# Kernel optimization log

Measured on AMD Instinct MI355X. Metric: run time of the kernel, lower is better.

The kernel has to match this reference:

```python
import jax, jax.numpy as jnp
import numpy as np

HIDDEN = 1024
N_HEAD = 16
LN_EPS = 1e-5


def _layernorm(x, g, b):
    m = jnp.mean(x, axis=-1, keepdims=True)
    v = jnp.var(x, axis=-1, keepdims=True)
    return (x - m) * jax.lax.rsqrt(v + LN_EPS) * g + b


def setup_inputs() -> dict:
    key = jax.random.key(0)
    ks = jax.random.split(key, 16)
    H = HIDDEN
    s = 0.02
    d = dict(
        x=jax.random.normal(ks[0], (4, 1024, H), jnp.float32),
        Wq=jax.random.normal(ks[1], (H, H), jnp.float32) * s,
        bq=jnp.zeros((H,), jnp.float32),
        Wk=jax.random.normal(ks[2], (H, H), jnp.float32) * s,
        bk=jnp.zeros((H,), jnp.float32),
        Wv=jax.random.normal(ks[3], (H, H), jnp.float32) * s,
        bv=jnp.zeros((H,), jnp.float32),
        Wo=jax.random.normal(ks[4], (H, H), jnp.float32) * s,
        bo=jnp.zeros((H,), jnp.float32),
        g1=jax.random.normal(ks[5], (H,), jnp.float32) * s,
        b1=jnp.zeros((H,), jnp.float32),
        W1=jax.random.normal(ks[6], (H, 4 * H), jnp.float32) * s,
        c1=jnp.zeros((4 * H,), jnp.float32),
        W2=jax.random.normal(ks[7], (4 * H, H), jnp.float32) * s,
        c2=jnp.zeros((H,), jnp.float32),
        g2=jax.random.normal(ks[8], (H,), jnp.float32) * s,
        b2=jnp.zeros((H,), jnp.float32),
    )
    return d


def reference(x, Wq, bq, Wk, bk, Wv, bv, Wo, bo, g1, b1, W1, c1, W2, c2, g2, b2):
    N, T, Hd = x.shape
    Hh = N_HEAD
    D = Hd // Hh
    # faithful to torch code: .view(N, H, T, D) is a raw reshape, no transpose
    q = (x @ Wq + bq).reshape(N, Hh, T, D)
    k = (x @ Wk + bk).reshape(N, Hh, T, D)
    v = (x @ Wv + bv).reshape(N, Hh, T, D)
    scores = jnp.einsum('nhtd,nhsd->nhts', q, k) / jnp.sqrt(jnp.float32(Hd))
    # faithful: softmax over dim=1 (the head axis)
    attn = jax.nn.softmax(scores, axis=1)
    o = jnp.einsum('nhts,nhsd->nhtd', attn, v).reshape(N, T, Hd)
    o = o @ Wo + bo
    x1 = _layernorm(o + x, g1, b1)
    ff = jax.nn.gelu(x1 @ W1 + c1, approximate=False) @ W2 + c2
    return _layernorm(ff + x1, g2, b2)
```

## Files before the change

kernel.cpp:

```cpp
#include <hip/hip_runtime.h>
#include <cstdint>
#include <cstddef>

#define EPI_QKV  0
#define EPI_F32  2
#define EPI_GELU 3
#define EPI_PART 4

typedef __attribute__((ext_vector_type(8))) short bfrag8;
typedef __attribute__((ext_vector_type(4))) float facc4;

struct PtrQuad { unsigned short* p[4]; };

__device__ __forceinline__ unsigned short f2b(float x) {
  unsigned int u = __builtin_bit_cast(unsigned int, x);
  u += 0x7FFFu + ((u >> 16) & 1u);
  return (unsigned short)(u >> 16);
}
__device__ __forceinline__ float b2f(unsigned short u) {
  unsigned int x = ((unsigned int)u) << 16;
  return __builtin_bit_cast(float, x);
}

__device__ __forceinline__ void gl2lds16(const unsigned short* g, unsigned short* l) {
  __builtin_amdgcn_global_load_lds(
      (const __attribute__((address_space(1))) unsigned int*)g,
      (__attribute__((address_space(3))) unsigned int*)l, 16, 0, 0);
}

__global__ __launch_bounds__(256)
void cvt_bf16_kernel(const float* __restrict__ in, unsigned short* __restrict__ out, int n4) {
  const int i = blockIdx.x * 256 + threadIdx.x;
  if (i < n4) {
    const float4 v = ((const float4*)in)[i];
    ushort4 u;
    u.x = f2b(v.x); u.y = f2b(v.y); u.z = f2b(v.z); u.w = f2b(v.w);
    ((ushort4*)out)[i] = u;
  }
}

__global__ __launch_bounds__(256)
void transpose_cvt(const float* __restrict__ in, unsigned short* __restrict__ out,
                   int K, int N) {
  __shared__ float tile[32][33];
  const int n0 = blockIdx.x * 32;
  const int k0 = blockIdx.y * 32;
  const int tx = threadIdx.x & 31, ty = threadIdx.x >> 5;
#pragma unroll
  for (int i = 0; i < 32; i += 8)
    tile[ty + i][tx] = in[(size_t)(k0 + ty + i) * N + n0 + tx];
  __syncthreads();
#pragma unroll
  for (int i = 0; i < 32; i += 8)
    out[(size_t)(n0 + ty + i) * K + k0 + tx] = f2b(tile[tx][ty + i]);
}

template<int EPI>
__global__ __launch_bounds__(256, 2)
void gemm_bt(const unsigned short* __restrict__ A,
             const unsigned short* __restrict__ Bt,
             const float* __restrict__ bias,
             const float* __restrict__ bias2,
             const float* __restrict__ bias3,
             void* __restrict__ out, PtrQuad pq,
             int M, int N, int K, int ldk) {
  __shared__ unsigned short sA[128 * 32];
  __shared__ unsigned short sB[128 * 32];
  const int tid  = threadIdx.x;
  const int lane = tid & 63;
  const int wave = tid >> 6;
  const int l15  = lane & 15, l4 = lane >> 4;
  const int wr = wave >> 1, wc = wave & 1;
  const long row0 = (long)blockIdx.y * 128;
  const long col0 = (long)blockIdx.x * 128;
  const long k0   = (long)blockIdx.z * K;

  facc4 acc[4][4];
#pragma unroll
  for (int i = 0; i < 4; i++)
#pragma unroll
    for (int j = 0; j < 4; j++) acc[i][j] = (facc4)0.f;

  const int srow = tid >> 2;
  const int scol = (tid & 3) * 8;
  const unsigned short* Ap0 = A  + (row0 + srow) * (long)ldk + k0 + scol;
  const unsigned short* Ap1 = Ap0 + 64 * (long)ldk;
  const unsigned short* Bp0 = Bt + (col0 + srow) * (long)ldk + k0 + scol;
  const unsigned short* Bp1 = Bp0 + 64 * (long)ldk;
  const int wbase = (tid & ~63) * 8;
  unsigned short* sA0 = &sA[wbase];
  unsigned short* sA1 = &sA[2048 + wbase];
  unsigned short* sB0 = &sB[wbase];
  unsigned short* sB1 = &sB[2048 + wbase];

  const int aoff = (wr * 64 + l15) * 32 + l4 * 8;
  const int boff = (wc * 64 + l15) * 32 + l4 * 8;

  for (int kt = 0; kt < K; kt += 32) {
    gl2lds16(Ap0 + kt, sA0);
    gl2lds16(Ap1 + kt, sA1);
    gl2lds16(Bp0 + kt, sB0);
    gl2lds16(Bp1 + kt, sB1);
    __syncthreads();
    bfrag8 af[4], bf[4];
#pragma unroll
    for (int i = 0; i < 4; i++) af[i] = *(const bfrag8*)&sA[aoff + i * 512];
#pragma unroll
    for (int j = 0; j < 4; j++) bf[j] = *(const bfrag8*)&sB[boff + j * 512];
#pragma unroll
    for (int i = 0; i < 4; i++)
#pragma unroll
      for (int j = 0; j < 4; j++)
        acc[i][j] = __builtin_amdgcn_mfma_f32_16x16x32_bf16(af[i], bf[j], acc[i][j], 0, 0, 0);
    __syncthreads();
  }

#pragma unroll
  for (int i = 0; i < 4; i++) {
    const long m0 = row0 + wr * 64 + i * 16 + l4 * 4;
#pragma unroll
    for (int j = 0; j < 4; j++) {
      const long c = col0 + wc * 64 + j * 16 + l15;
      if constexpr (EPI == EPI_QKV) {
        const long which = c >> 10;
        const long cl = c & 1023;
        unsigned short* oq = (unsigned short*)out;
        if (which == 0) {
          const float bj = bias[cl];
#pragma unroll
          for (int r = 0; r < 4; r++)
            oq[(m0 + r) * 1024 + cl] = f2b((acc[i][j][r] + bj) * 0.03125f);
        } else if (which == 1) {
          const float bj = bias2[cl];
#pragma unroll
          for (int r = 0; r < 4; r++)
            (oq + 4194304)[(m0 + r) * 1024 + cl] = f2b(acc[i][j][r] + bj);
        } else {
          const float bj = bias3[cl];
          const long cc = cl >> 6, d = cl & 63;
#pragma unroll
          for (int r = 0; r < 4; r++) {
            const long m = m0 + r;
            const long nbb = m >> 10, rr = m & 1023;
            const long h = rr >> 6, rhi = rr & 63;
            const long s = rhi * 16 + cc;
            (oq + 8388608)[((nbb * 16 + h) * 64 + d) * 1024 + s] = f2b(acc[i][j][r] + bj);
          }
        }
      } else if constexpr (EPI == EPI_F32) {
        const float bj = bias[c];
        float* of = (float*)out;
#pragma unroll
        for (int r = 0; r < 4; r++) of[(m0 + r) * (long)N + c] = acc[i][j][r] + bj;
      } else if constexpr (EPI == EPI_PART) {
        unsigned short* ob = pq.p[blockIdx.z];
#pragma unroll
        for (int r = 0; r < 4; r++) ob[(m0 + r) * (long)N + c] = f2b(acc[i][j][r]);
      } else {
        const float bj = bias[c];
        unsigned short* ob = (unsigned short*)out;
#pragma unroll
        for (int r = 0; r < 4; r++) {
          const float t = acc[i][j][r] + bj;
          ob[(m0 + r) * (long)N + c] = f2b(0.5f * t * (1.f + erff(t * 0.70710678f)));
        }
      }
    }
  }
}

__global__ __launch_bounds__(512, 4)
void attn_kernel(const unsigned short* __restrict__ Qb,
                 const unsigned short* __restrict__ Kb,
                 const unsigned short* __restrict__ Vt,
                 unsigned short* __restrict__ P0, unsigned short* __restrict__ P1) {
  const int id = blockIdx.x;
  const int combo = id & 7;
  const int tile = id >> 3;
  const int nb = combo & 3;
  const int sp = combo >> 2;
  const int tid = threadIdx.x, lane = tid & 63;
  const int w = __builtin_amdgcn_readfirstlane(tid >> 6);
  const int l15 = lane & 15, l4 = lane >> 4;
  const int t0 = tile * 16;

  __shared__ float red[2][8][576];
  __shared__ __align__(16) unsigned short abuf[8][16][40];

  const size_t hb0 = (size_t)(nb * 16 + w * 2) << 16;
  const unsigned short* qB = Qb + hb0;
  const unsigned short* kB = Kb + hb0;
  const unsigned short* vB = Vt + hb0;

  bfrag8 qf[2][2];
#pragma unroll
  for (int hh = 0; hh < 2; hh++)
#pragma unroll
    for (int ks = 0; ks < 2; ks++)
      qf[hh][ks] = *(const bfrag8*)(qB + (hh << 16) + (t0 + l15) * 64 + ks * 32 + l4 * 8);

  facc4 oacc[2][4];
#pragma unroll
  for (int hh = 0; hh < 2; hh++)
#pragma unroll
    for (int nt = 0; nt < 4; nt++) oacc[hh][nt] = (facc4)0.f;

  for (int it = 0; it < 16; ++it) {
    const int s0 = sp * 512 + it * 32;
    const int pb = it & 1;
    facc4 sacc[2][2];
#pragma unroll
    for (int hh = 0; hh < 2; hh++)
#pragma unroll
      for (int nt = 0; nt < 2; nt++) sacc[hh][nt] = (facc4)0.f;
#pragma unroll
    for (int hh = 0; hh < 2; hh++) {
      const unsigned short* kh = kB + (hh << 16);
#pragma unroll
      for (int ks = 0; ks < 2; ks++)
#pragma unroll
        for (int nt = 0; nt < 2; nt++) {
          const bfrag8 kf = *(const bfrag8*)(kh + (s0 + nt * 16 + l15) * 64 + ks * 32 + l4 * 8);
          sacc[hh][nt] = __builtin_amdgcn_mfma_f32_16x16x32_bf16(qf[hh][ks], kf, sacc[hh][nt], 0, 0, 0);
        }
    }
    bfrag8 vf0[4], vf1[4];
#pragma unroll
    for (int nt = 0; nt < 4; nt++) {
      vf0[nt] = *(const bfrag8*)(vB + (size_t)(nt * 16 + l15) * 1024 + s0 + l4 * 8);
      vf1[nt] = *(const bfrag8*)(vB + (1 << 16) + (size_t)(nt * 16 + l15) * 1024 + s0 + l4 * 8);
    }
#pragma unroll
    for (int nt = 0; nt < 2; nt++)
#pragma unroll
      for (int r = 0; r < 4; r++) {
        const float e0 = __expf(sacc[0][nt][r]);
        const float e1 = __expf(sacc[1][nt][r]);
        sacc[0][nt][r] = e0; sacc[1][nt][r] = e1;
        red[pb][w][(l4 * 4 + r) * 36 + nt * 16 + l15] = e0 + e1;
      }
    __syncthreads();
    float rinv[2][4];
#pragma unroll
    for (int nt = 0; nt < 2; nt++)
#pragma unroll
      for (int r = 0; r < 4; r++) {
        const int o = (l4 * 4 + r) * 36 + nt * 16 + l15;
        float s = 0.f;
#pragma unroll
        for (int ww = 0; ww < 8; ww++) s += red[pb][ww][o];
        rinv[nt][r] = 1.f / s;
      }
#pragma unroll
    for (int nt = 0; nt < 2; nt++)
#pragma unroll
      for (int r = 0; r < 4; r++)
        abuf[w][l4 * 4 + r][nt * 16 + l15] = f2b(sacc[0][nt][r] * rinv[nt][r]);
    {
      const bfrag8 af0 = *(const bfrag8*)&abuf[w][l15][l4 * 8];
#pragma unroll
      for (int nt = 0; nt < 4; nt++)
        oacc[0][nt] = __builtin_amdgcn_mfma_f32_16x16x32_bf16(af0, vf0[nt], oacc[0][nt], 0, 0, 0);
    }
#pragma unroll
    for (int nt = 0; nt < 2; nt++)
#pragma unroll
      for (int r = 0; r < 4; r++)
        abuf[w][l4 * 4 + r][nt * 16 + l15] = f2b(sacc[1][nt][r] * rinv[nt][r]);
    {
      const bfrag8 af1 = *(const bfrag8*)&abuf[w][l15][l4 * 8];
#pragma unroll
      for (int nt = 0; nt < 4; nt++)
        oacc[1][nt] = __builtin_amdgcn_mfma_f32_16x16x32_bf16(af1, vf1[nt], oacc[1][nt], 0, 0, 0);
    }
  }
  unsigned short* P = sp ? P1 : P0;
#pragma unroll
  for (int hh = 0; hh < 2; hh++) {
    const size_t rb = ((size_t)nb * 1024 + (size_t)(w * 2 + hh) * 64 + tile) * 1024;
#pragma unroll
    for (int nt = 0; nt < 4; nt++)
#pragma unroll
      for (int r = 0; r < 4; r++)
        P[rb + (size_t)(l4 * 4 + r) * 64 + nt * 16 + l15] = f2b(oacc[hh][nt][r]);
  }
}

__global__ __launch_bounds__(256)
void reduce_o2(const unsigned short* __restrict__ P0, const unsigned short* __restrict__ P1,
               unsigned short* __restrict__ OB, int n4) {
  const int i = blockIdx.x * 256 + threadIdx.x;
  if (i < n4) {
    const ushort4 a = ((const ushort4*)P0)[i];
    const ushort4 b = ((const ushort4*)P1)[i];
    ushort4 u;
    u.x = f2b(b2f(a.x) + b2f(b.x));
    u.y = f2b(b2f(a.y) + b2f(b.y));
    u.z = f2b(b2f(a.z) + b2f(b.z));
    u.w = f2b(b2f(a.w) + b2f(b.w));
    ((ushort4*)OB)[i] = u;
  }
}

__global__ __launch_bounds__(256)
void ln_red(const unsigned short* __restrict__ P0, const unsigned short* __restrict__ P1,
            const unsigned short* __restrict__ P2, const unsigned short* __restrict__ P3,
            const float* __restrict__ bias, const float* __restrict__ resid,
            const float* __restrict__ g, const float* __restrict__ be,
            float* __restrict__ outf, unsigned short* __restrict__ outb) {
  const int row = blockIdx.x, tid = threadIdx.x;
  const size_t o4 = (size_t)row * 256 + tid;
  const ushort4 a = ((const ushort4*)P0)[o4];
  const ushort4 b = ((const ushort4*)P1)[o4];
  const ushort4 c = ((const ushort4*)P2)[o4];
  const ushort4 d = ((const ushort4*)P3)[o4];
  const float4 vb = ((const float4*)bias)[tid];
  const float4 vr = ((const float4*)resid)[o4];
  float t0 = b2f(a.x) + b2f(b.x) + b2f(c.x) + b2f(d.x) + vb.x + vr.x;
  float t1 = b2f(a.y) + b2f(b.y) + b2f(c.y) + b2f(d.y) + vb.y + vr.y;
  float t2 = b2f(a.z) + b2f(b.z) + b2f(c.z) + b2f(d.z) + vb.z + vr.z;
  float t3 = b2f(a.w) + b2f(b.w) + b2f(c.w) + b2f(d.w) + vb.w + vr.w;
  float s = t0 + t1 + t2 + t3;
  float q = t0 * t0 + t1 * t1 + t2 * t2 + t3 * t3;
#pragma unroll
  for (int off = 32; off > 0; off >>= 1) {
    s += __shfl_down(s, off, 64);
    q += __shfl_down(q, off, 64);
  }
  __shared__ float rs_[4], rq_[4];
  if ((tid & 63) == 0) { rs_[tid >> 6] = s; rq_[tid >> 6] = q; }
  __syncthreads();
  const float S = rs_[0] + rs_[1] + rs_[2] + rs_[3];
  const float Q = rq_[0] + rq_[1] + rq_[2] + rq_[3];
  const float mean = S * (1.f / 1024.f);
  const float var  = Q * (1.f / 1024.f) - mean * mean;
  const float rstd = rsqrtf(var + 1e-5f);
  const float4 vg  = ((const float4*)g)[tid];
  const float4 vbe = ((const float4*)be)[tid];
  float o0 = (t0 - mean) * rstd * vg.x + vbe.x;
  float o1 = (t1 - mean) * rstd * vg.y + vbe.y;
  float o2 = (t2 - mean) * rstd * vg.z + vbe.z;
  float o3 = (t3 - mean) * rstd * vg.w + vbe.w;
  ((float4*)(outf + (size_t)row * 1024))[tid] = make_float4(o0, o1, o2, o3);
  if (outb != nullptr) {
    ushort4 u;
    u.x = f2b(o0); u.y = f2b(o1); u.z = f2b(o2); u.w = f2b(o3);
    ((ushort4*)(outb + (size_t)row * 1024))[tid] = u;
  }
}

extern "C" void kernel_launch(void* const* d_in, const int* in_sizes, int n_in,
                              void* d_out, int out_size, void* d_ws, size_t ws_size,
                              hipStream_t stream) {
  const float* x  = (const float*)d_in[0];
  const float* Wq = (const float*)d_in[1];
  const float* bq = (const float*)d_in[2];
  const float* Wk = (const float*)d_in[3];
  const float* bk = (const float*)d_in[4];
  const float* Wv = (const float*)d_in[5];
  const float* bv = (const float*)d_in[6];
  const float* Wo = (const float*)d_in[7];
  const float* bo = (const float*)d_in[8];
  const float* g1 = (const float*)d_in[9];
  const float* b1 = (const float*)d_in[10];
  const float* W1 = (const float*)d_in[11];
  const float* c1 = (const float*)d_in[12];
  const float* W2 = (const float*)d_in[13];
  const float* c2 = (const float*)d_in[14];
  const float* g2 = (const float*)d_in[15];
  const float* b2 = (const float*)d_in[16];
  float* out = (float*)d_out;

  char* ws = (char*)d_ws;
  unsigned short* XB  = (unsigned short*)(ws);
  unsigned short* WQT = (unsigned short*)(ws + 8388608);
  unsigned short* WKT = (unsigned short*)(ws + 10485760);
  unsigned short* WVT = (unsigned short*)(ws + 12582912);
  unsigned short* WOT = (unsigned short*)(ws + 14680064);
  unsigned short* W1T = (unsigned short*)(ws + 16777216);
  unsigned short* W2T = (unsigned short*)(ws + 25165824);
  float*          X1  = (float*)(ws + 33554432);
  unsigned short* X1B = (unsigned short*)(ws + 50331648);
  char* RB = ws + 58720256;
  unsigned short* QB  = (unsigned short*)(RB);
  unsigned short* KB  = (unsigned short*)(RB + 8388608);
  unsigned short* VT  = (unsigned short*)(RB + 16777216);
  unsigned short* OB  = (unsigned short*)(RB + 25165824);
  unsigned short* H1B = (unsigned short*)(RB);
  unsigned short* AP0 = (unsigned short*)(RB + 33554432);
  unsigned short* AP1 = (unsigned short*)(RB + 41943040);
  PtrQuad OPQ = { { QB, KB, VT, XB } };
  PtrQuad FPQ = { { XB, X1B, (unsigned short*)(RB + 33554432),
                    (unsigned short*)(RB + 41943040) } };
  PtrQuad ZQ = { { nullptr, nullptr, nullptr, nullptr } };

  const dim3 tb(256);
  cvt_bf16_kernel<<<dim3(4096), tb, 0, stream>>>(x, XB, 1048576);
  transpose_cvt<<<dim3(32, 32),  tb, 0, stream>>>(Wq, WQT, 1024, 1024);
  transpose_cvt<<<dim3(32, 32),  tb, 0, stream>>>(Wk, WKT, 1024, 1024);
  transpose_cvt<<<dim3(32, 32),  tb, 0, stream>>>(Wv, WVT, 1024, 1024);
  transpose_cvt<<<dim3(32, 32),  tb, 0, stream>>>(Wo, WOT, 1024, 1024);
  transpose_cvt<<<dim3(128, 32), tb, 0, stream>>>(W1, W1T, 1024, 4096);
  transpose_cvt<<<dim3(32, 128), tb, 0, stream>>>(W2, W2T, 4096, 1024);
  gemm_bt<EPI_QKV><<<dim3(24, 32), tb, 0, stream>>>(XB, WQT, bq, bk, bv, (void*)QB, ZQ,
                                                    4096, 3072, 1024, 1024);
  attn_kernel<<<dim3(512), dim3(512), 0, stream>>>(QB, KB, VT, AP0, AP1);
  reduce_o2<<<dim3(4096), tb, 0, stream>>>(AP0, AP1, OB, 1048576);
  gemm_bt<EPI_PART><<<dim3(8, 32, 4), tb, 0, stream>>>(OB, WOT, nullptr, nullptr, nullptr,
                                                       nullptr, OPQ, 4096, 1024, 256, 1024);
  ln_red<<<dim3(4096), tb, 0, stream>>>(QB, KB, VT, XB, bo, x, g1, b1, X1, X1B);
  gemm_bt<EPI_GELU><<<dim3(32, 32), tb, 0, stream>>>(X1B, W1T, c1, nullptr, nullptr,
                                                     (void*)H1B, ZQ, 4096, 4096, 1024, 1024);
  gemm_bt<EPI_PART><<<dim3(8, 32, 4), tb, 0, stream>>>(H1B, W2T, nullptr, nullptr, nullptr,
                                                       nullptr, FPQ, 4096, 1024, 1024, 4096);
  ln_red<<<dim3(4096), tb, 0, stream>>>(FPQ.p[0], FPQ.p[1], FPQ.p[2], FPQ.p[3], c2, X1,
                                        g2, b2, out, (unsigned short*)nullptr);
}
```

Before: 463.0 us.

## Restructure head-axis softmax attention to keep all heads per wave in registers

The attention kernel is reorganised so each wave computes scores for all 16 heads over its own 16-key slice, and the head-axis softmax is reduced entirely in registers instead of through a cross-wave LDS reduction. Q for a 32-row tile is staged once into swizzled LDS and reused across heads. Normalised probabilities are exchanged through an LDS buffer so each wave can run P·V for its two heads over a 128-key step. Tiles double to 32 query rows and the grid is halved, which raises register pressure (occupancy hint lowered to 2) and adds several barriers per iteration.

```diff
diff --git a/kernel.cpp b/kernel.cpp
--- a/kernel.cpp
+++ b/kernel.cpp
@@ -169,120 +169,161 @@
   }
 }
 
-__global__ __launch_bounds__(512, 4)
+__global__ __launch_bounds__(512, 2)
 void attn_kernel(const unsigned short* __restrict__ Qb,
                  const unsigned short* __restrict__ Kb,
                  const unsigned short* __restrict__ Vt,
                  unsigned short* __restrict__ P0, unsigned short* __restrict__ P1) {
   const int id = blockIdx.x;
   const int combo = id & 7;
-  const int tile = id >> 3;
   const int nb = combo & 3;
   const int sp = combo >> 2;
+  const int tile = id >> 3;
   const int tid = threadIdx.x, lane = tid & 63;
   const int w = __builtin_amdgcn_readfirstlane(tid >> 6);
   const int l15 = lane & 15, l4 = lane >> 4;
-  const int t0 = tile * 16;
-
-  __shared__ float red[2][8][576];
-  __shared__ __align__(16) unsigned short abuf[8][16][40];
-
-  const size_t hb0 = (size_t)(nb * 16 + w * 2) << 16;
-  const unsigned short* qB = Qb + hb0;
-  const unsigned short* kB = Kb + hb0;
-  const unsigned short* vB = Vt + hb0;
-
-  bfrag8 qf[2][2];
+  const int t0 = tile * 32;
+  const int sbase = sp * 512;
+
+  __shared__ __align__(16) unsigned short Qs[16 * 32 * 64];
+  __shared__ __align__(16) unsigned short Ps[16 * 16 * 128];
+
+  const size_t bb = ((size_t)(nb * 16)) << 16;
+  const unsigned short* qB = Qb + bb;
+  const unsigned short* kB = Kb + bb;
+  const unsigned short* vB = Vt + bb;
+
+#pragma unroll
+  for (int kk = 0; kk < 8; kk++) {
+    const int j = kk * 512 + tid;
+    const int h = j >> 8, t = (j >> 3) & 31, d8 = j & 7;
+    const int4 v = *(const int4*)(qB + ((size_t)h << 16) + (size_t)(t0 + t) * 64 + d8 * 8);
+    *(int4*)((char*)Qs + h * 4096 + t * 128 + ((d8 * 16) ^ ((t & 7) << 4))) = v;
+  }
+
+  const int swz = (l15 & 7) << 4;
+  const int qrA = l15 * 128;
+  const int qrB = (16 + l15) * 128;
+  const int qo0 = (l4 * 16) ^ swz;
+  const int qo1 = (64 + l4 * 16) ^ swz;
+  const int pwb = l15 * 256 + (((w * 16 + l4 * 4) * 2) ^ swz);
+  int pro[4];
+#pragma unroll
+  for (int ks = 0; ks < 4; ks++) pro[ks] = l15 * 256 + ((ks * 64 + l4 * 16) ^ swz);
+
+  const int h0 = w * 2;
+  facc4 oacc[2][2][4];
 #pragma unroll
   for (int hh = 0; hh < 2; hh++)
 #pragma unroll
-    for (int ks = 0; ks < 2; ks++)
-      qf[hh][ks] = *(const bfrag8*)(qB + (hh << 16) + (t0 + l15) * 64 + ks * 32 + l4 * 8);
-
-  facc4 oacc[2][4];
-#pragma unroll
-  for (int hh = 0; hh < 2; hh++)
-#pragma unroll
-    for (int nt = 0; nt < 4; nt++) oacc[hh][nt] = (facc4)0.f;
-
-  for (int it = 0; it < 16; ++it) {
-    const int s0 = sp * 512 + it * 32;
-    const int pb = it & 1;
-    facc4 sacc[2][2];
+    for (int st = 0; st < 2; st++)
+#pragma unroll
+      for (int nt = 0; nt < 4; nt++) oacc[hh][st][nt] = (facc4)0.f;
+
+  __syncthreads();
+
+  for (int it = 0; it < 4; ++it) {
+    const int s0w = sbase + it * 128 + w * 16;
+    facc4 scA[16], scB[16];
+#pragma unroll
+    for (int h = 0; h < 16; h++) {
+      const unsigned short* kh = kB + ((size_t)h << 16) + (size_t)(s0w + l15) * 64 + l4 * 8;
+      const bfrag8 kf0 = *(const bfrag8*)kh;
+      const bfrag8 kf1 = *(const bfrag8*)(kh + 32);
+      const char* qh = (const char*)Qs + h * 4096;
+      const bfrag8 qA0 = *(const bfrag8*)(qh + qrA + qo0);
+      const bfrag8 qA1 = *(const bfrag8*)(qh + qrA + qo1);
+      const bfrag8 qB0 = *(const bfrag8*)(qh + qrB + qo0);
+      const bfrag8 qB1 = *(const bfrag8*)(qh + qrB + qo1);
+      facc4 a = __builtin_amdgcn_mfma_f32_16x16x32_bf16(kf0, qA0, (facc4)0.f, 0, 0, 0);
+      scA[h] = __builtin_amdgcn_mfma_f32_16x16x32_bf16(kf1, qA1, a, 0, 0, 0);
+      facc4 b = __builtin_amdgcn_mfma_f32_16x16x32_bf16(kf0, qB0, (facc4)0.f, 0, 0, 0);
+      scB[h] = __builtin_amdgcn_mfma_f32_16x16x32_bf16(kf1, qB1, b, 0, 0, 0);
+    }
+    {
+      float d0 = 0.f, d1 = 0.f, d2 = 0.f, d3 = 0.f;
+#pragma unroll
+      for (int h = 0; h < 16; h++) {
+        scA[h][0] = __expf(scA[h][0]); d0 += scA[h][0];
+        scA[h][1] = __expf(scA[h][1]); d1 += scA[h][1];
+        scA[h][2] = __expf(scA[h][2]); d2 += scA[h][2];
+        scA[h][3] = __expf(scA[h][3]); d3 += scA[h][3];
+      }
+      const float r0 = 1.f / d0, r1 = 1.f / d1, r2 = 1.f / d2, r3 = 1.f / d3;
+#pragma unroll
+      for (int h = 0; h < 16; h++) {
+        const float p0 = scA[h][0] * r0, p1 = scA[h][1] * r1;
+        const float p2 = scA[h][2] * r2, p3 = scA[h][3] * r3;
+        uint2 pk;
+        asm("v_cvt_pk_bf16_f32 %0, %1, %2" : "=v"(pk.x) : "v"(p0), "v"(p1));
+        asm("v_cvt_pk_bf16_f32 %0, %1, %2" : "=v"(pk.y) : "v"(p2), "v"(p3));
+        *(uint2*)((char*)Ps + h * 4096 + pwb) = pk;
+      }
+    }
+    __syncthreads();
+    bfrag8 afA[2][4];
 #pragma unroll
     for (int hh = 0; hh < 2; hh++)
 #pragma unroll
-      for (int nt = 0; nt < 2; nt++) sacc[hh][nt] = (facc4)0.f;
+      for (int ks = 0; ks < 4; ks++)
+        afA[hh][ks] = *(const bfrag8*)((char*)Ps + (h0 + hh) * 4096 + pro[ks]);
+    __syncthreads();
+    {
+      float d0 = 0.f, d1 = 0.f, d2 = 0.f, d3 = 0.f;
+#pragma unroll
+      for (int h = 0; h < 16; h++) {
+        scB[h][0] = __expf(scB[h][0]); d0 += scB[h][0];
+        scB[h][1] = __expf(scB[h][1]); d1 += scB[h][1];
+        scB[h][2] = __expf(scB[h][2]); d2 += scB[h][2];
+        scB[h][3] = __expf(scB[h][3]); d3 += scB[h][3];
+      }
+      const float r0 = 1.f / d0, r1 = 1.f / d1, r2 = 1.f / d2, r3 = 1.f / d3;
+#pragma unroll
+      for (int h = 0; h < 16; h++) {
+        const float p0 = scB[h][0] * r0, p1 = scB[h][1] * r1;
+        const float p2 = scB[h][2] * r2, p3 = scB[h][3] * r3;
+        uint2 pk;
+        asm("v_cvt_pk_bf16_f32 %0, %1, %2" : "=v"(pk.x) : "v"(p0), "v"(p1));
+        asm("v_cvt_pk_bf16_f32 %0, %1, %2" : "=v"(pk.y) : "v"(p2), "v"(p3));
+        *(uint2*)((char*)Ps + h * 4096 + pwb) = pk;
+      }
+    }
+    __syncthreads();
+    bfrag8 afB[2][4];
+#pragma unroll
+    for (int hh = 0; hh < 2; hh++)
+#pragma unroll
+      for (int ks = 0; ks < 4; ks++)
+        afB[hh][ks] = *(const bfrag8*)((char*)Ps + (h0 + hh) * 4096 + pro[ks]);
+    __syncthreads();
 #pragma unroll
     for (int hh = 0; hh < 2; hh++) {
-      const unsigned short* kh = kB + (hh << 16);
-#pragma unroll
-      for (int ks = 0; ks < 2; ks++)
-#pragma unroll
-        for (int nt = 0; nt < 2; nt++) {
-          const bfrag8 kf = *(const bfrag8*)(kh + (s0 + nt * 16 + l15) * 64 + ks * 32 + l4 * 8);
-          sacc[hh][nt] = __builtin_amdgcn_mfma_f32_16x16x32_bf16(qf[hh][ks], kf, sacc[hh][nt], 0, 0, 0);
+      const unsigned short* vh = vB + ((size_t)(h0 + hh) << 16) + sbase + it * 128 + l4 * 8;
+#pragma unroll
+      for (int ks = 0; ks < 4; ks++)
+#pragma unroll
+        for (int nt = 0; nt < 4; nt++) {
+          const bfrag8 vf = *(const bfrag8*)(vh + (size_t)(nt * 16 + l15) * 1024 + ks * 32);
+          oacc[hh][0][nt] =
+              __builtin_amdgcn_mfma_f32_16x16x32_bf16(afA[hh][ks], vf, oacc[hh][0][nt], 0, 0, 0);
+          oacc[hh][1][nt] =
+              __builtin_amdgcn_mfma_f32_16x16x32_bf16(afB[hh][ks], vf, oacc[hh][1][nt], 0, 0, 0);
         }
     }
-    bfrag8 vf0[4], vf1[4];
-#pragma unroll
-    for (int nt = 0; nt < 4; nt++) {
-      vf0[nt] = *(const bfrag8*)(vB + (size_t)(nt * 16 + l15) * 1024 + s0 + l4 * 8);
-      vf1[nt] = *(const bfrag8*)(vB + (1 << 16) + (size_t)(nt * 16 + l15) * 1024 + s0 + l4 * 8);
-    }
-#pragma unroll
-    for (int nt = 0; nt < 2; nt++)
-#pragma unroll
-      for (int r = 0; r < 4; r++) {
-        const float e0 = __expf(sacc[0][nt][r]);
-        const float e1 = __expf(sacc[1][nt][r]);
-        sacc[0][nt][r] = e0; sacc[1][nt][r] = e1;
-        red[pb][w][(l4 * 4 + r) * 36 + nt * 16 + l15] = e0 + e1;
-      }
-    __syncthreads();
-    float rinv[2][4];
-#pragma unroll
-    for (int nt = 0; nt < 2; nt++)
-#pragma unroll
-      for (int r = 0; r < 4; r++) {
-        const int o = (l4 * 4 + r) * 36 + nt * 16 + l15;
-        float s = 0.f;
-#pragma unroll
-        for (int ww = 0; ww < 8; ww++) s += red[pb][ww][o];
-        rinv[nt][r] = 1.f / s;
-      }
-#pragma unroll
-    for (int nt = 0; nt < 2; nt++)
-#pragma unroll
-      for (int r = 0; r < 4; r++)
-        abuf[w][l4 * 4 + r][nt * 16 + l15] = f2b(sacc[0][nt][r] * rinv[nt][r]);
-    {
-      const bfrag8 af0 = *(const bfrag8*)&abuf[w][l15][l4 * 8];
+  }
+
+  unsigned short* P = sp ? P1 : P0;
+#pragma unroll
+  for (int hh = 0; hh < 2; hh++) {
+    const size_t hb = ((size_t)nb << 20) + ((size_t)(h0 + hh) << 16);
+#pragma unroll
+    for (int st = 0; st < 2; st++)
 #pragma unroll
       for (int nt = 0; nt < 4; nt++)
-        oacc[0][nt] = __builtin_amdgcn_mfma_f32_16x16x32_bf16(af0, vf0[nt], oacc[0][nt], 0, 0, 0);
-    }
-#pragma unroll
-    for (int nt = 0; nt < 2; nt++)
-#pragma unroll
-      for (int r = 0; r < 4; r++)
-        abuf[w][l4 * 4 + r][nt * 16 + l15] = f2b(sacc[1][nt][r] * rinv[nt][r]);
-    {
-      const bfrag8 af1 = *(const bfrag8*)&abuf[w][l15][l4 * 8];
-#pragma unroll
-      for (int nt = 0; nt < 4; nt++)
-        oacc[1][nt] = __builtin_amdgcn_mfma_f32_16x16x32_bf16(af1, vf1[nt], oacc[1][nt], 0, 0, 0);
-    }
-  }
-  unsigned short* P = sp ? P1 : P0;
-#pragma unroll
-  for (int hh = 0; hh < 2; hh++) {
-    const size_t rb = ((size_t)nb * 1024 + (size_t)(w * 2 + hh) * 64 + tile) * 1024;
-#pragma unroll
-    for (int nt = 0; nt < 4; nt++)
-#pragma unroll
-      for (int r = 0; r < 4; r++)
-        P[rb + (size_t)(l4 * 4 + r) * 64 + nt * 16 + l15] = f2b(oacc[hh][nt][r]);
+#pragma unroll
+        for (int r = 0; r < 4; r++)
+          P[hb + (size_t)(t0 + st * 16 + l4 * 4 + r) * 64 + nt * 16 + l15] =
+              f2b(oacc[hh][st][nt][r]);
   }
 }
 
@@ -404,7 +445,7 @@
   transpose_cvt<<<dim3(32, 128), tb, 0, stream>>>(W2, W2T, 4096, 1024);
   gemm_bt<EPI_QKV><<<dim3(24, 32), tb, 0, stream>>>(XB, WQT, bq, bk, bv, (void*)QB, ZQ,
                                                     4096, 3072, 1024, 1024);
-  attn_kernel<<<dim3(512), dim3(512), 0, stream>>>(QB, KB, VT, AP0, AP1);
+  attn_kernel<<<dim3(256), dim3(512), 0, stream>>>(QB, KB, VT, AP0, AP1);
   reduce_o2<<<dim3(4096), tb, 0, stream>>>(AP0, AP1, OB, 1048576);
   gemm_bt<EPI_PART><<<dim3(8, 32, 4), tb, 0, stream>>>(OB, WOT, nullptr, nullptr, nullptr,
                                                        nullptr, OPQ, 4096, 1024, 256, 1024);
```

After: 423.4 us. -8.5%, faster.

## Restructure attention kernel with head-split QK and LDS-staged probabilities

Applied to the files above, without the earlier changes.

Reorganizes the attention kernel so each warp computes scores for 8 heads over a 16-key sub-slice, and Q is staged once in swizzled LDS. The head-axis softmax denominator is combined across just two warp groups instead of eight. Probabilities are packed to bf16 with a hardware convert instruction and exchanged through LDS so each warp then runs PV for its own 2 heads over 64 keys per iteration. This halves the iteration count and cuts reduction traffic, at the cost of an extra barrier per iteration and larger LDS use. The output write indexing also changes, which may alter the layout handed to the reduction stage.

```diff
diff --git a/kernel.cpp b/kernel.cpp
--- a/kernel.cpp
+++ b/kernel.cpp
@@ -176,113 +176,124 @@
                  unsigned short* __restrict__ P0, unsigned short* __restrict__ P1) {
   const int id = blockIdx.x;
   const int combo = id & 7;
-  const int tile = id >> 3;
   const int nb = combo & 3;
   const int sp = combo >> 2;
+  const int tile = id >> 3;
   const int tid = threadIdx.x, lane = tid & 63;
   const int w = __builtin_amdgcn_readfirstlane(tid >> 6);
   const int l15 = lane & 15, l4 = lane >> 4;
   const int t0 = tile * 16;
-
-  __shared__ float red[2][8][576];
-  __shared__ __align__(16) unsigned short abuf[8][16][40];
-
-  const size_t hb0 = (size_t)(nb * 16 + w * 2) << 16;
-  const unsigned short* qB = Qb + hb0;
-  const unsigned short* kB = Kb + hb0;
-  const unsigned short* vB = Vt + hb0;
-
-  bfrag8 qf[2][2];
+  const int sbase = sp * 512;
+
+  __shared__ __align__(16) unsigned short Qs[16 * 16 * 64];
+  __shared__ __align__(16) unsigned short Ps[16 * 16 * 64];
+  __shared__ __align__(16) float Ds[2 * 16 * 64];
+
+  const size_t bb = ((size_t)(nb * 16)) << 16;
+  const unsigned short* qB = Qb + bb;
+  const unsigned short* kB = Kb + bb;
+  const unsigned short* vB = Vt + bb;
+
+#pragma unroll
+  for (int kk = 0; kk < 4; kk++) {
+    const int j = kk * 512 + tid;
+    const int h = j >> 7, t = (j >> 3) & 15, d8 = j & 7;
+    const int4 v = *(const int4*)(qB + ((size_t)h << 16) + (size_t)(t0 + t) * 64 + d8 * 8);
+    *(int4*)((char*)Qs + h * 2048 + t * 128 + ((d8 * 16) ^ ((t & 7) << 4))) = v;
+  }
+
+  const int g   = w & 1;
+  const int sw  = w >> 1;
+  const int h0q = g * 8;
+  const int hpv = w * 2;
+  const int swz = (l15 & 7) << 4;
+
+  const int qrow = l15 * 128;
+  const int qo0 = (l4 * 16) ^ swz;
+  const int qo1 = (64 + l4 * 16) ^ swz;
+  const int pwb = l15 * 128 + ((sw * 32 + l4 * 8) ^ swz);
+  const int pr0 = l15 * 128 + ((l4 * 16) ^ swz);
+  const int pr1 = l15 * 128 + ((64 + l4 * 16) ^ swz);
+  const int dwo = l15 * 256 + ((sw * 64 + l4 * 16) ^ swz);
+
+  facc4 oacc[2][4];
 #pragma unroll
   for (int hh = 0; hh < 2; hh++)
 #pragma unroll
-    for (int ks = 0; ks < 2; ks++)
-      qf[hh][ks] = *(const bfrag8*)(qB + (hh << 16) + (t0 + l15) * 64 + ks * 32 + l4 * 8);
-
-  facc4 oacc[2][4];
-#pragma unroll
-  for (int hh = 0; hh < 2; hh++)
-#pragma unroll
     for (int nt = 0; nt < 4; nt++) oacc[hh][nt] = (facc4)0.f;
 
-  for (int it = 0; it < 16; ++it) {
-    const int s0 = sp * 512 + it * 32;
-    const int pb = it & 1;
-    facc4 sacc[2][2];
-#pragma unroll
-    for (int hh = 0; hh < 2; hh++)
-#pragma unroll
-      for (int nt = 0; nt < 2; nt++) sacc[hh][nt] = (facc4)0.f;
+  __syncthreads();
+
+  for (int it = 0; it < 8; ++it) {
+    const int s0 = sbase + it * 64;
+    const int sW = s0 + sw * 16;
+    facc4 sc[8];
+#pragma unroll
+    for (int hi = 0; hi < 8; hi++) {
+      const int h = h0q + hi;
+      const unsigned short* kh = kB + ((size_t)h << 16) + (size_t)(sW + l15) * 64 + l4 * 8;
+      const bfrag8 kf0 = *(const bfrag8*)kh;
+      const bfrag8 kf1 = *(const bfrag8*)(kh + 32);
+      const char* qh = (const char*)Qs + h * 2048 + qrow;
+      const bfrag8 q0 = *(const bfrag8*)(qh + qo0);
+      const bfrag8 q1 = *(const bfrag8*)(qh + qo1);
+      facc4 a = __builtin_amdgcn_mfma_f32_16x16x32_bf16(kf0, q0, (facc4)0.f, 0, 0, 0);
+      sc[hi] = __builtin_amdgcn_mfma_f32_16x16x32_bf16(kf1, q1, a, 0, 0, 0);
+    }
+    float d0 = 0.f, d1 = 0.f, d2 = 0.f, d3 = 0.f;
+#pragma unroll
+    for (int hi = 0; hi < 8; hi++) {
+      sc[hi][0] = __expf(sc[hi][0]); d0 += sc[hi][0];
+      sc[hi][1] = __expf(sc[hi][1]); d1 += sc[hi][1];
+      sc[hi][2] = __expf(sc[hi][2]); d2 += sc[hi][2];
+      sc[hi][3] = __expf(sc[hi][3]); d3 += sc[hi][3];
+    }
+    *(float4*)((char*)Ds + g * 4096 + dwo) = make_float4(d0, d1, d2, d3);
+    __syncthreads();
+    const float4 dp = *(const float4*)((char*)Ds + (g ^ 1) * 4096 + dwo);
+    const float r0 = 1.f / (d0 + dp.x);
+    const float r1 = 1.f / (d1 + dp.y);
+    const float r2 = 1.f / (d2 + dp.z);
+    const float r3 = 1.f / (d3 + dp.w);
+#pragma unroll
+    for (int hi = 0; hi < 8; hi++) {
+      const float p0 = sc[hi][0] * r0, p1 = sc[hi][1] * r1;
+      const float p2 = sc[hi][2] * r2, p3 = sc[hi][3] * r3;
+      uint2 pk;
+      asm("v_cvt_pk_bf16_f32 %0, %1, %2" : "=v"(pk.x) : "v"(p0), "v"(p1));
+      asm("v_cvt_pk_bf16_f32 %0, %1, %2" : "=v"(pk.y) : "v"(p2), "v"(p3));
+      *(uint2*)((char*)Ps + (h0q + hi) * 2048 + pwb) = pk;
+    }
+    __syncthreads();
+    bfrag8 af[2][2];
 #pragma unroll
     for (int hh = 0; hh < 2; hh++) {
-      const unsigned short* kh = kB + (hh << 16);
+      af[hh][0] = *(const bfrag8*)((char*)Ps + (hpv + hh) * 2048 + pr0);
+      af[hh][1] = *(const bfrag8*)((char*)Ps + (hpv + hh) * 2048 + pr1);
+    }
+#pragma unroll
+    for (int hh = 0; hh < 2; hh++) {
+      const unsigned short* vh = vB + ((size_t)(hpv + hh) << 16) + s0 + l4 * 8;
 #pragma unroll
       for (int ks = 0; ks < 2; ks++)
 #pragma unroll
-        for (int nt = 0; nt < 2; nt++) {
-          const bfrag8 kf = *(const bfrag8*)(kh + (s0 + nt * 16 + l15) * 64 + ks * 32 + l4 * 8);
-          sacc[hh][nt] = __builtin_amdgcn_mfma_f32_16x16x32_bf16(qf[hh][ks], kf, sacc[hh][nt], 0, 0, 0);
+        for (int nt = 0; nt < 4; nt++) {
+          const bfrag8 vf = *(const bfrag8*)(vh + (size_t)(nt * 16 + l15) * 1024 + ks * 32);
+          oacc[hh][nt] =
+              __builtin_amdgcn_mfma_f32_16x16x32_bf16(af[hh][ks], vf, oacc[hh][nt], 0, 0, 0);
         }
     }
-    bfrag8 vf0[4], vf1[4];
-#pragma unroll
-    for (int nt = 0; nt < 4; nt++) {
-      vf0[nt] = *(const bfrag8*)(vB + (size_t)(nt * 16 + l15) * 1024 + s0 + l4 * 8);
-      vf1[nt] = *(const bfrag8*)(vB + (1 << 16) + (size_t)(nt * 16 + l15) * 1024 + s0 + l4 * 8);
-    }
-#pragma unroll
-    for (int nt = 0; nt < 2; nt++)
-#pragma unroll
-      for (int r = 0; r < 4; r++) {
-        const float e0 = __expf(sacc[0][nt][r]);
-        const float e1 = __expf(sacc[1][nt][r]);
-        sacc[0][nt][r] = e0; sacc[1][nt][r] = e1;
-        red[pb][w][(l4 * 4 + r) * 36 + nt * 16 + l15] = e0 + e1;
-      }
-    __syncthreads();
-    float rinv[2][4];
-#pragma unroll
-    for (int nt = 0; nt < 2; nt++)
-#pragma unroll
-      for (int r = 0; r < 4; r++) {
-        const int o = (l4 * 4 + r) * 36 + nt * 16 + l15;
-        float s = 0.f;
-#pragma unroll
-        for (int ww = 0; ww < 8; ww++) s += red[pb][ww][o];
-        rinv[nt][r] = 1.f / s;
-      }
-#pragma unroll
-    for (int nt = 0; nt < 2; nt++)
+  }
+
+  unsigned short* P = sp ? P1 : P0;
+#pragma unroll
+  for (int hh = 0; hh < 2; hh++) {
+    const size_t hb = ((size_t)nb << 20) + ((size_t)(hpv + hh) << 16);
+#pragma unroll
+    for (int nt = 0; nt < 4; nt++)
 #pragma unroll
       for (int r = 0; r < 4; r++)
-        abuf[w][l4 * 4 + r][nt * 16 + l15] = f2b(sacc[0][nt][r] * rinv[nt][r]);
-    {
-      const bfrag8 af0 = *(const bfrag8*)&abuf[w][l15][l4 * 8];
-#pragma unroll
-      for (int nt = 0; nt < 4; nt++)
-        oacc[0][nt] = __builtin_amdgcn_mfma_f32_16x16x32_bf16(af0, vf0[nt], oacc[0][nt], 0, 0, 0);
-    }
-#pragma unroll
-    for (int nt = 0; nt < 2; nt++)
-#pragma unroll
-      for (int r = 0; r < 4; r++)
-        abuf[w][l4 * 4 + r][nt * 16 + l15] = f2b(sacc[1][nt][r] * rinv[nt][r]);
-    {
-      const bfrag8 af1 = *(const bfrag8*)&abuf[w][l15][l4 * 8];
-#pragma unroll
-      for (int nt = 0; nt < 4; nt++)
-        oacc[1][nt] = __builtin_amdgcn_mfma_f32_16x16x32_bf16(af1, vf1[nt], oacc[1][nt], 0, 0, 0);
-    }
-  }
-  unsigned short* P = sp ? P1 : P0;
-#pragma unroll
-  for (int hh = 0; hh < 2; hh++) {
-    const size_t rb = ((size_t)nb * 1024 + (size_t)(w * 2 + hh) * 64 + tile) * 1024;
-#pragma unroll
-    for (int nt = 0; nt < 4; nt++)
-#pragma unroll
-      for (int r = 0; r < 4; r++)
-        P[rb + (size_t)(l4 * 4 + r) * 64 + nt * 16 + l15] = f2b(oacc[hh][nt][r]);
+        P[hb + (size_t)(t0 + l4 * 4 + r) * 64 + nt * 16 + l15] = f2b(oacc[hh][nt][r]);
   }
 }
 
```

After: 461.5 us. Within noise of the previous version (-0.3%).

## Restructure attention kernel: 4 heads per wave, 64-row tiles, 4-way key split

Applied to the files above, without the earlier changes.

The attention kernel is reorganised so each wave handles 4 heads and 32 query rows. Blocks now cover 64 query rows with a 4-way split over keys instead of 2-way, which gives 256 blocks. The head-axis softmax denominator is partly summed in registers and only reduced across 4 head groups through LDS, instead of across 8 waves. The bf16 packing uses v_cvt_pk_bf16_f32 with an XOR-swizzled LDS layout, and the final reduction now sums 4 partial outputs. This is meant to increase reuse of loaded K/V fragments and cut LDS reduction traffic. In exchange it raises register pressure (launch bounds drop to 1 block), halves the grid, adds extra partial-buffer traffic, and reuses workspace regions (X1 area) for the partials.

```diff
diff --git a/kernel.cpp b/kernel.cpp
--- a/kernel.cpp
+++ b/kernel.cpp
@@ -169,135 +169,193 @@
   }
 }
 
-__global__ __launch_bounds__(512, 4)
+__global__ __launch_bounds__(512, 1)
 void attn_kernel(const unsigned short* __restrict__ Qb,
                  const unsigned short* __restrict__ Kb,
                  const unsigned short* __restrict__ Vt,
-                 unsigned short* __restrict__ P0, unsigned short* __restrict__ P1) {
+                 PtrQuad APQ) {
   const int id = blockIdx.x;
-  const int combo = id & 7;
-  const int tile = id >> 3;
+  const int combo = id & 15;
   const int nb = combo & 3;
   const int sp = combo >> 2;
+  const int tile = id >> 4;
   const int tid = threadIdx.x, lane = tid & 63;
   const int w = __builtin_amdgcn_readfirstlane(tid >> 6);
   const int l15 = lane & 15, l4 = lane >> 4;
-  const int t0 = tile * 16;
-
-  __shared__ float red[2][8][576];
-  __shared__ __align__(16) unsigned short abuf[8][16][40];
-
-  const size_t hb0 = (size_t)(nb * 16 + w * 2) << 16;
-  const unsigned short* qB = Qb + hb0;
-  const unsigned short* kB = Kb + hb0;
-  const unsigned short* vB = Vt + hb0;
-
-  bfrag8 qf[2][2];
-#pragma unroll
-  for (int hh = 0; hh < 2; hh++)
-#pragma unroll
-    for (int ks = 0; ks < 2; ks++)
-      qf[hh][ks] = *(const bfrag8*)(qB + (hh << 16) + (t0 + l15) * 64 + ks * 32 + l4 * 8);
-
-  facc4 oacc[2][4];
-#pragma unroll
-  for (int hh = 0; hh < 2; hh++)
-#pragma unroll
-    for (int nt = 0; nt < 4; nt++) oacc[hh][nt] = (facc4)0.f;
-
-  for (int it = 0; it < 16; ++it) {
-    const int s0 = sp * 512 + it * 32;
-    const int pb = it & 1;
-    facc4 sacc[2][2];
-#pragma unroll
-    for (int hh = 0; hh < 2; hh++)
-#pragma unroll
-      for (int nt = 0; nt < 2; nt++) sacc[hh][nt] = (facc4)0.f;
-#pragma unroll
-    for (int hh = 0; hh < 2; hh++) {
-      const unsigned short* kh = kB + (hh << 16);
-#pragma unroll
-      for (int ks = 0; ks < 2; ks++)
-#pragma unroll
-        for (int nt = 0; nt < 2; nt++) {
-          const bfrag8 kf = *(const bfrag8*)(kh + (s0 + nt * 16 + l15) * 64 + ks * 32 + l4 * 8);
-          sacc[hh][nt] = __builtin_amdgcn_mfma_f32_16x16x32_bf16(qf[hh][ks], kf, sacc[hh][nt], 0, 0, 0);
-        }
-    }
-    bfrag8 vf0[4], vf1[4];
-#pragma unroll
-    for (int nt = 0; nt < 4; nt++) {
-      vf0[nt] = *(const bfrag8*)(vB + (size_t)(nt * 16 + l15) * 1024 + s0 + l4 * 8);
-      vf1[nt] = *(const bfrag8*)(vB + (1 << 16) + (size_t)(nt * 16 + l15) * 1024 + s0 + l4 * 8);
-    }
-#pragma unroll
-    for (int nt = 0; nt < 2; nt++)
-#pragma unroll
-      for (int r = 0; r < 4; r++) {
-        const float e0 = __expf(sacc[0][nt][r]);
-        const float e1 = __expf(sacc[1][nt][r]);
-        sacc[0][nt][r] = e0; sacc[1][nt][r] = e1;
-        red[pb][w][(l4 * 4 + r) * 36 + nt * 16 + l15] = e0 + e1;
+  const int tg = w >> 2;
+  const int hg = w & 3;
+  const int t0 = tile * 64 + tg * 32;
+  const int h0 = hg * 4;
+  const int sbase = sp * 256;
+
+  __shared__ float Ds[2][2][4][32][33];
+  __shared__ __align__(16) unsigned short Pw[8][8][512];
+
+  const size_t bb = ((size_t)(nb * 16)) << 16;
+  const unsigned short* qB = Qb + bb;
+  const unsigned short* kB = Kb + bb;
+  const unsigned short* vB = Vt + bb;
+
+  bfrag8 qf[4][2][2];
+#pragma unroll
+  for (int hi = 0; hi < 4; hi++)
+#pragma unroll
+    for (int ts = 0; ts < 2; ts++)
+#pragma unroll
+      for (int dh = 0; dh < 2; dh++)
+        qf[hi][ts][dh] = *(const bfrag8*)(qB + ((size_t)(h0 + hi) << 16)
+            + (size_t)(t0 + ts * 16 + l15) * 64 + dh * 32 + l4 * 8);
+
+  facc4 oacc[4][2][4];
+#pragma unroll
+  for (int hi = 0; hi < 4; hi++)
+#pragma unroll
+    for (int ts = 0; ts < 2; ts++)
+#pragma unroll
+      for (int nt = 0; nt < 4; nt++) oacc[hi][ts][nt] = (facc4)0.f;
+
+  const int pswz = (l15 & 3) << 4;
+  char* pw = (char*)&Pw[w][0][0];
+
+  for (int it = 0; it < 8; ++it) {
+    const int s0 = sbase + it * 32;
+    bfrag8 kf[4][2][2];
+#pragma unroll
+    for (int hi = 0; hi < 4; hi++)
+#pragma unroll
+      for (int ss = 0; ss < 2; ss++)
+#pragma unroll
+        for (int dh = 0; dh < 2; dh++)
+          kf[hi][ss][dh] = *(const bfrag8*)(kB + ((size_t)(h0 + hi) << 16)
+              + (size_t)(s0 + ss * 16 + l15) * 64 + dh * 32 + l4 * 8);
+    facc4 sc[4][2][2];
+#pragma unroll
+    for (int hi = 0; hi < 4; hi++)
+#pragma unroll
+      for (int ts = 0; ts < 2; ts++)
+#pragma unroll
+        for (int ss = 0; ss < 2; ss++) {
+          facc4 a = __builtin_amdgcn_mfma_f32_16x16x32_bf16(kf[hi][ss][0], qf[hi][ts][0],
+                                                            (facc4)0.f, 0, 0, 0);
+          sc[hi][ts][ss] = __builtin_amdgcn_mfma_f32_16x16x32_bf16(kf[hi][ss][1],
+                                                                   qf[hi][ts][1], a, 0, 0, 0);
+        }
+    bfrag8 vf[4][4];
+#pragma unroll
+    for (int hi = 0; hi < 4; hi++)
+#pragma unroll
+      for (int nt = 0; nt < 4; nt++)
+        vf[hi][nt] = *(const bfrag8*)(vB + ((size_t)(h0 + hi) << 16)
+            + (size_t)(nt * 16 + l15) * 1024 + s0 + l4 * 8);
+    float dp[2][2][4];
+#pragma unroll
+    for (int ts = 0; ts < 2; ts++)
+#pragma unroll
+      for (int ss = 0; ss < 2; ss++)
+#pragma unroll
+        for (int r = 0; r < 4; r++) dp[ts][ss][r] = 0.f;
+#pragma unroll
+    for (int hi = 0; hi < 4; hi++)
+#pragma unroll
+      for (int ts = 0; ts < 2; ts++)
+#pragma unroll
+        for (int ss = 0; ss < 2; ss++)
+#pragma unroll
+          for (int r = 0; r < 4; r++) {
+            const float e = __expf(sc[hi][ts][ss][r]);
+            sc[hi][ts][ss][r] = e;
+            dp[ts][ss][r] += e;
+          }
+    const int p = it & 1;
+#pragma unroll
+    for (int ts = 0; ts < 2; ts++)
+#pragma unroll
+      for (int ss = 0; ss < 2; ss++)
+#pragma unroll
+        for (int r = 0; r < 4; r++)
+          Ds[p][tg][hg][ss * 16 + l4 * 4 + r][ts * 16 + l15] = dp[ts][ss][r];
+    __syncthreads();
+    float ri[2][2][4];
+#pragma unroll
+    for (int ts = 0; ts < 2; ts++)
+#pragma unroll
+      for (int ss = 0; ss < 2; ss++)
+#pragma unroll
+        for (int r = 0; r < 4; r++) {
+          const int si = ss * 16 + l4 * 4 + r;
+          const int ti = ts * 16 + l15;
+          float s = dp[ts][ss][r];
+          s += Ds[p][tg][(hg + 1) & 3][si][ti];
+          s += Ds[p][tg][(hg + 2) & 3][si][ti];
+          s += Ds[p][tg][(hg + 3) & 3][si][ti];
+          ri[ts][ss][r] = 1.f / s;
+        }
+#pragma unroll
+    for (int hi = 0; hi < 4; hi++)
+#pragma unroll
+      for (int ts = 0; ts < 2; ts++) {
+        uint2 a, b;
+        {
+          const float p0 = sc[hi][ts][0][0] * ri[ts][0][0];
+          const float p1 = sc[hi][ts][0][1] * ri[ts][0][1];
+          const float p2 = sc[hi][ts][0][2] * ri[ts][0][2];
+          const float p3 = sc[hi][ts][0][3] * ri[ts][0][3];
+          asm("v_cvt_pk_bf16_f32 %0, %1, %2" : "=v"(a.x) : "v"(p0), "v"(p1));
+          asm("v_cvt_pk_bf16_f32 %0, %1, %2" : "=v"(a.y) : "v"(p2), "v"(p3));
+        }
+        {
+          const float p0 = sc[hi][ts][1][0] * ri[ts][1][0];
+          const float p1 = sc[hi][ts][1][1] * ri[ts][1][1];
+          const float p2 = sc[hi][ts][1][2] * ri[ts][1][2];
+          const float p3 = sc[hi][ts][1][3] * ri[ts][1][3];
+          asm("v_cvt_pk_bf16_f32 %0, %1, %2" : "=v"(b.x) : "v"(p0), "v"(p1));
+          asm("v_cvt_pk_bf16_f32 %0, %1, %2" : "=v"(b.y) : "v"(p2), "v"(p3));
+        }
+        char* base = pw + (hi * 2 + ts) * 1024 + l15 * 64;
+        *(uint2*)(base + ((l4 * 8) ^ pswz)) = a;
+        *(uint2*)(base + ((32 + l4 * 8) ^ pswz)) = b;
       }
-    __syncthreads();
-    float rinv[2][4];
-#pragma unroll
-    for (int nt = 0; nt < 2; nt++)
-#pragma unroll
-      for (int r = 0; r < 4; r++) {
-        const int o = (l4 * 4 + r) * 36 + nt * 16 + l15;
-        float s = 0.f;
-#pragma unroll
-        for (int ww = 0; ww < 8; ww++) s += red[pb][ww][o];
-        rinv[nt][r] = 1.f / s;
+#pragma unroll
+    for (int hi = 0; hi < 4; hi++)
+#pragma unroll
+      for (int ts = 0; ts < 2; ts++) {
+        const bfrag8 af = *(const bfrag8*)(pw + (hi * 2 + ts) * 1024 + l15 * 64
+                                           + ((l4 * 16) ^ pswz));
+#pragma unroll
+        for (int nt = 0; nt < 4; nt++)
+          oacc[hi][ts][nt] = __builtin_amdgcn_mfma_f32_16x16x32_bf16(af, vf[hi][nt],
+                                                                     oacc[hi][ts][nt], 0, 0, 0);
       }
-#pragma unroll
-    for (int nt = 0; nt < 2; nt++)
-#pragma unroll
-      for (int r = 0; r < 4; r++)
-        abuf[w][l4 * 4 + r][nt * 16 + l15] = f2b(sacc[0][nt][r] * rinv[nt][r]);
-    {
-      const bfrag8 af0 = *(const bfrag8*)&abuf[w][l15][l4 * 8];
+  }
+
+  unsigned short* P = APQ.p[sp];
+#pragma unroll
+  for (int hi = 0; hi < 4; hi++) {
+    const size_t hb = ((size_t)nb << 20) + ((size_t)(h0 + hi) << 16);
+#pragma unroll
+    for (int ts = 0; ts < 2; ts++)
 #pragma unroll
       for (int nt = 0; nt < 4; nt++)
-        oacc[0][nt] = __builtin_amdgcn_mfma_f32_16x16x32_bf16(af0, vf0[nt], oacc[0][nt], 0, 0, 0);
-    }
-#pragma unroll
-    for (int nt = 0; nt < 2; nt++)
-#pragma unroll
-      for (int r = 0; r < 4; r++)
-        abuf[w][l4 * 4 + r][nt * 16 + l15] = f2b(sacc[1][nt][r] * rinv[nt][r]);
-    {
-      const bfrag8 af1 = *(const bfrag8*)&abuf[w][l15][l4 * 8];
-#pragma unroll
-      for (int nt = 0; nt < 4; nt++)
-        oacc[1][nt] = __builtin_amdgcn_mfma_f32_16x16x32_bf16(af1, vf1[nt], oacc[1][nt], 0, 0, 0);
-    }
-  }
-  unsigned short* P = sp ? P1 : P0;
-#pragma unroll
-  for (int hh = 0; hh < 2; hh++) {
-    const size_t rb = ((size_t)nb * 1024 + (size_t)(w * 2 + hh) * 64 + tile) * 1024;
-#pragma unroll
-    for (int nt = 0; nt < 4; nt++)
-#pragma unroll
-      for (int r = 0; r < 4; r++)
-        P[rb + (size_t)(l4 * 4 + r) * 64 + nt * 16 + l15] = f2b(oacc[hh][nt][r]);
+#pragma unroll
+        for (int r = 0; r < 4; r++)
+          P[hb + (size_t)(t0 + ts * 16 + l4 * 4 + r) * 64 + nt * 16 + l15] =
+              f2b(oacc[hi][ts][nt][r]);
   }
 }
 
 __global__ __launch_bounds__(256)
-void reduce_o2(const unsigned short* __restrict__ P0, const unsigned short* __restrict__ P1,
-               unsigned short* __restrict__ OB, int n4) {
+void reduce_o4(PtrQuad pq, unsigned short* __restrict__ OB, int n4) {
   const int i = blockIdx.x * 256 + threadIdx.x;
   if (i < n4) {
-    const ushort4 a = ((const ushort4*)P0)[i];
-    const ushort4 b = ((const ushort4*)P1)[i];
+    const ushort4 a = ((const ushort4*)pq.p[0])[i];
+    const ushort4 b = ((const ushort4*)pq.p[1])[i];
+    const ushort4 c = ((const ushort4*)pq.p[2])[i];
+    const ushort4 d = ((const ushort4*)pq.p[3])[i];
     ushort4 u;
-    u.x = f2b(b2f(a.x) + b2f(b.x));
-    u.y = f2b(b2f(a.y) + b2f(b.y));
-    u.z = f2b(b2f(a.z) + b2f(b.z));
-    u.w = f2b(b2f(a.w) + b2f(b.w));
+    u.x = f2b(b2f(a.x) + b2f(b.x) + b2f(c.x) + b2f(d.x));
+    u.y = f2b(b2f(a.y) + b2f(b.y) + b2f(c.y) + b2f(d.y));
+    u.z = f2b(b2f(a.z) + b2f(b.z) + b2f(c.z) + b2f(d.z));
+    u.w = f2b(b2f(a.w) + b2f(b.w) + b2f(c.w) + b2f(d.w));
     ((ushort4*)OB)[i] = u;
   }
 }
@@ -389,6 +447,9 @@
   unsigned short* H1B = (unsigned short*)(RB);
   unsigned short* AP0 = (unsigned short*)(RB + 33554432);
   unsigned short* AP1 = (unsigned short*)(RB + 41943040);
+  unsigned short* AP2 = (unsigned short*)(ws + 33554432);
+  unsigned short* AP3 = (unsigned short*)(ws + 41943040);
+  PtrQuad APQ = { { AP0, AP1, AP2, AP3 } };
   PtrQuad OPQ = { { QB, KB, VT, XB } };
   PtrQuad FPQ = { { XB, X1B, (unsigned short*)(RB + 33554432),
                     (unsigned short*)(RB + 41943040) } };
@@ -404,8 +465,8 @@
   transpose_cvt<<<dim3(32, 128), tb, 0, stream>>>(W2, W2T, 4096, 1024);
   gemm_bt<EPI_QKV><<<dim3(24, 32), tb, 0, stream>>>(XB, WQT, bq, bk, bv, (void*)QB, ZQ,
                                                     4096, 3072, 1024, 1024);
-  attn_kernel<<<dim3(512), dim3(512), 0, stream>>>(QB, KB, VT, AP0, AP1);
-  reduce_o2<<<dim3(4096), tb, 0, stream>>>(AP0, AP1, OB, 1048576);
+  attn_kernel<<<dim3(256), dim3(512), 0, stream>>>(QB, KB, VT, APQ);
+  reduce_o4<<<dim3(4096), tb, 0, stream>>>(APQ, OB, 1048576);
   gemm_bt<EPI_PART><<<dim3(8, 32, 4), tb, 0, stream>>>(OB, WOT, nullptr, nullptr, nullptr,
                                                        nullptr, OPQ, 4096, 1024, 256, 1024);
   ln_red<<<dim3(4096), tb, 0, stream>>>(QB, KB, VT, XB, bo, x, g1, b1, X1, X1B);
```

New measurement: 494.4 us. 1.07x slower.
